# Kernel optimization log

Hardware: AMD Instinct MI355X
Metric: run time of the kernel (lower is better)

The kernel has to match this reference:

```python
import jax, jax.numpy as jnp
import numpy as np
from jax.scipy import special

B, N, DIM, H, DK, DV, F = 2, 1536, 1536, 8, 64, 64, 192


def _pos_embed(seq_len, feat):
    """Enformer relative positional basis: [2*seq_len-1, feat]."""
    per = feat // 6  # 3 basis families x (symmetric, antisymmetric)
    d = jnp.arange(-seq_len + 1, seq_len, dtype=jnp.float32)
    ad = jnp.abs(d)[:, None]  # [2N-1, 1]
    # exponential decay, log-spaced half lives
    half_life = 2.0 ** jnp.linspace(3.0, float(np.log2(seq_len)), per)
    expo = jnp.exp(-jnp.log(2.0) / half_life * ad)
    # central binary mask
    widths = 2.0 ** jnp.arange(1, per + 1, dtype=jnp.float32) - 1.0
    cmask = (widths > ad).astype(jnp.float32)
    # gamma pdf basis
    stddev = seq_len / (2.0 * per)
    start_mean = seq_len / per
    mean = jnp.linspace(start_mean, float(seq_len), per)
    conc = (mean / stddev) ** 2
    rate = mean / stddev ** 2
    log_unnorm = special.xlogy(conc - 1.0, ad) - rate * ad
    log_norm = special.gammaln(conc) - conc * jnp.log(rate)
    probs = jnp.exp(log_unnorm - log_norm) + 1e-8
    gamma = probs / jnp.max(probs, axis=-1, keepdims=True)
    emb = jnp.concatenate([expo, cmask, gamma], axis=-1)
    emb = jnp.concatenate([emb, jnp.sign(d)[:, None] * emb], axis=-1)
    return emb.astype(jnp.float32)


def _relative_shift(x):
    # x: [B, H, N, 2N-1] -> [B, H, N, N] (Transformer-XL shift)
    b, h, t1, t2 = x.shape
    x = jnp.pad(x, ((0, 0), (0, 0), (0, 0), (1, 0)))  # [B,H,N,2N]
    x = x.reshape(b, h, t2 + 1, t1)[:, :, 1:, :].reshape(b, h, t1, t2)
    return x[..., : (t2 + 2) // 2]


def setup_inputs() -> dict:
    key = jax.random.key(0)
    ks = jax.random.split(key, 8)
    s = 0.02
    return {
        "x": jax.random.normal(ks[0], (B, N, DIM), dtype=jnp.float32),
        "Wq": jax.random.normal(ks[1], (DIM, H * DK), dtype=jnp.float32) * s,
        "Wk": jax.random.normal(ks[2], (DIM, H * DK), dtype=jnp.float32) * s,
        "Wv": jax.random.normal(ks[3], (DIM, H * DV), dtype=jnp.float32) * s,
        "Wrel": jax.random.normal(ks[4], (F, H * DK), dtype=jnp.float32) * s,
        "Wout": jax.random.normal(ks[5], (H * DV, DIM), dtype=jnp.float32) * s,
        "bout": jnp.zeros((DIM,), dtype=jnp.float32),
        "rel_content_bias": jax.random.normal(ks[6], (1, H, 1, DK), dtype=jnp.float32),
        "rel_pos_bias": jax.random.normal(ks[7], (1, H, 1, DK), dtype=jnp.float32),
        "pos_embed": _pos_embed(N, F),  # [2N-1, F] buffer
    }


def reference(x, Wq, Wk, Wv, Wrel, Wout, bout, rel_content_bias, rel_pos_bias, pos_embed):
    b, n, _ = x.shape
    h, dk = rel_content_bias.shape[1], rel_content_bias.shape[3]
    dv = Wv.shape[1] // h
    scale = dk ** -0.5
    q = (x @ Wq).reshape(b, n, h, dk).transpose(0, 2, 1, 3) * scale  # [b,h,n,dk]
    k = (x @ Wk).reshape(b, n, h, dk).transpose(0, 2, 1, 3)
    v = (x @ Wv).reshape(b, n, h, dv).transpose(0, 2, 1, 3)
    content_logits = jnp.einsum('bhid,bhjd->bhij', q + rel_content_bias, k)
    rel_k = (pos_embed @ Wrel).reshape(-1, h, dk).transpose(1, 0, 2)  # [h,2n-1,dk]
    rel_logits = jnp.einsum('bhid,hjd->bhij', q + rel_pos_bias, rel_k)  # [b,h,n,2n-1]
    rel_logits = _relative_shift(rel_logits)  # [b,h,n,n]
    attn = jax.nn.softmax(content_logits + rel_logits, axis=-1)
    out = jnp.einsum('bhij,bhjd->bhid', attn, v)
    out = out.transpose(0, 2, 1, 3).reshape(b, n, h * dv)
    return out @ Wout + bout
```

## Files before the change

kernel.cpp:

```cpp
#include <hip/hip_runtime.h>

#define NSEQ  1536
#define HEADS 8
#define NREL  3071
#define NRELP 3072

typedef __bf16 bf16;
typedef __bf16 bf16x8 __attribute__((ext_vector_type(8)));
typedef __bf16 bf16x4 __attribute__((ext_vector_type(4)));
typedef float  f32x4  __attribute__((ext_vector_type(4)));

static __device__ __forceinline__ f32x4 mfma16(bf16x8 a, bf16x8 b, f32x4 c) {
  return __builtin_amdgcn_mfma_f32_16x16x32_bf16(a, b, c, 0, 0, 0);
}

static __device__ __forceinline__ void gload_lds16(const bf16* g, bf16* l) {
  __builtin_amdgcn_global_load_lds((const __attribute__((address_space(1))) void*)g,
                                   (__attribute__((address_space(3))) void*)l, 16, 0, 0);
}

#define DPP_F(v, ctrl) __int_as_float(__builtin_amdgcn_update_dpp(0, __float_as_int(v), ctrl, 0xF, 0xF, true))
static __device__ __forceinline__ float rowsum16(float v) {
  v += DPP_F(v, 0xB1);
  v += DPP_F(v, 0x4E);
  v += DPP_F(v, 0x124);
  v += DPP_F(v, 0x128);
  return v;
}

__global__ __launch_bounds__(256) void prep(const float* __restrict__ x, const float* __restrict__ pos,
                                            const float* __restrict__ Wq, const float* __restrict__ Wk,
                                            const float* __restrict__ Wv, const float* __restrict__ Wout,
                                            const float* __restrict__ Wrel,
                                            bf16* __restrict__ xb, bf16* __restrict__ posb,
                                            bf16* __restrict__ WT, bf16* __restrict__ WoT,
                                            bf16* __restrict__ WrT) {
  int blk = blockIdx.x;
  if (blk < 4608) {
    int i = blk * 256 + threadIdx.x;
    float4 v = ((const float4*)x)[i];
    bf16x4 o;
    o[0] = (bf16)v.x; o[1] = (bf16)v.y; o[2] = (bf16)v.z; o[3] = (bf16)v.w;
    ((bf16x4*)xb)[i] = o;
    return;
  }
  blk -= 4608;
  if (blk < 576) {
    int i = blk * 256 + threadIdx.x;
    if (i < (NREL * 192 / 4)) {
      float4 v = ((const float4*)pos)[i];
      bf16x4 o;
      o[0] = (bf16)v.x; o[1] = (bf16)v.y; o[2] = (bf16)v.z; o[3] = (bf16)v.w;
      ((bf16x4*)posb)[i] = o;
    }
    return;
  }
  blk -= 576;
  const float* in; bf16* out; int C, ostride, orowoff, cx, ry;
  if (blk < 768)       { in = Wq;   out = WT;  C = 512;  ostride = 1536; orowoff = 0;    cx = blk % 16; ry = blk / 16; }
  else if (blk < 1536) { blk -= 768;  in = Wk;   out = WT;  C = 512;  ostride = 1536; orowoff = 512;  cx = blk % 16; ry = blk / 16; }
  else if (blk < 2304) { blk -= 1536; in = Wv;   out = WT;  C = 512;  ostride = 1536; orowoff = 1024; cx = blk % 16; ry = blk / 16; }
  else if (blk < 3072) { blk -= 2304; in = Wout; out = WoT; C = 1536; ostride = 512;  orowoff = 0;    cx = blk % 48; ry = blk / 48; }
  else                 { blk -= 3072; in = Wrel; out = WrT; C = 512;  ostride = 192;  orowoff = 0;    cx = blk % 16; ry = blk / 16; }
  __shared__ float t[32][33];
  int tx = threadIdx.x & 31, ty = threadIdx.x >> 5;
  int r0 = ry * 32, c0 = cx * 32;
#pragma unroll
  for (int i = 0; i < 4; i++)
    t[ty + 8 * i][tx] = in[(size_t)(r0 + ty + 8 * i) * C + c0 + tx];
  __syncthreads();
#pragma unroll
  for (int i = 0; i < 4; i++)
    out[(size_t)(c0 + ty + 8 * i + orowoff) * ostride + r0 + tx] = (bf16)t[tx][ty + 8 * i];
}

static __device__ __forceinline__ void gemm_core(const bf16* __restrict__ A, const bf16* __restrict__ BT,
                                                 int Klen, int ldk, int m0, int n0, int M,
                                                 bf16* sa, bf16* sb, f32x4 acc[4][2]) {
  int tid = threadIdx.x, wave = tid >> 6, lane = tid & 63;
  int l15 = lane & 15, quad = lane >> 4;
  int lrow = lane >> 3, lcg = lane & 7;
  int swz = (lcg ^ lrow) * 8;

  int rowA = wave * 16 + lrow;
  int ra0 = m0 + rowA;     if (ra0 > M - 1) ra0 = M - 1;
  int ra1 = m0 + rowA + 8; if (ra1 > M - 1) ra1 = M - 1;
  const bf16* pA0 = A + (size_t)ra0 * ldk + swz;
  const bf16* pA1 = A + (size_t)ra1 * ldk + swz;
  int rowB = wave * 32 + lrow;
  const bf16* pB = BT + (size_t)(n0 + rowB) * ldk + swz;
  size_t ldk8 = (size_t)ldk * 8;
  bf16* wA = sa + rowA * 64 + lcg * 8;
  bf16* wB = sb + rowB * 64 + lcg * 8;

  float4 a0 = *(const float4*)pA0;
  float4 a1 = *(const float4*)pA1;
  float4 b0 = *(const float4*)(pB);
  float4 b1 = *(const float4*)(pB + ldk8);
  float4 b2 = *(const float4*)(pB + 2 * ldk8);
  float4 b3 = *(const float4*)(pB + 3 * ldk8);

  int swzA = (quad ^ (l15 & 7)) * 8;
  int swzB = ((4 + quad) ^ (l15 & 7)) * 8;

  for (int k0 = 0; k0 < Klen; k0 += 64) {
    __syncthreads();
    *(float4*)(wA) = a0;        *(float4*)(wA + 512) = a1;
    *(float4*)(wB) = b0;        *(float4*)(wB + 512) = b1;
    *(float4*)(wB + 1024) = b2; *(float4*)(wB + 1536) = b3;
    __syncthreads();
    if (k0 + 64 < Klen) {
      pA0 += 64; pA1 += 64; pB += 64;
      a0 = *(const float4*)pA0;
      a1 = *(const float4*)pA1;
      b0 = *(const float4*)(pB);
      b1 = *(const float4*)(pB + ldk8);
      b2 = *(const float4*)(pB + 2 * ldk8);
      b3 = *(const float4*)(pB + 3 * ldk8);
    }
#pragma unroll
    for (int kq = 0; kq < 2; kq++) {
      bf16x8 af[4], bfr[2];
      int sz = kq ? swzB : swzA;
#pragma unroll
      for (int rt = 0; rt < 4; rt++)
        af[rt] = *(const bf16x8*)&sa[(rt * 16 + l15) * 64 + sz];
#pragma unroll
      for (int ct = 0; ct < 2; ct++)
        bfr[ct] = *(const bf16x8*)&sb[(wave * 32 + ct * 16 + l15) * 64 + sz];
#pragma unroll
      for (int ct = 0; ct < 2; ct++)
#pragma unroll
        for (int rt = 0; rt < 4; rt++)
          acc[rt][ct] = mfma16(af[rt], bfr[ct], acc[rt][ct]);
    }
  }
}

__global__ __launch_bounds__(256) void gemm_qkvrel(const bf16* __restrict__ xb, const bf16* __restrict__ WT,
                                                   const bf16* __restrict__ posb, const bf16* __restrict__ WrT,
                                                   const float* __restrict__ cb, const float* __restrict__ pb,
                                                   bf16* __restrict__ qc, bf16* __restrict__ qp,
                                                   bf16* __restrict__ kb, bf16* __restrict__ vt,
                                                   bf16* __restrict__ rk) {
  __shared__ __align__(16) bf16 sa[64 * 64];
  __shared__ __align__(16) bf16 sb[128 * 64];
  __shared__ __align__(16) bf16 tv[64 * 130];
  int tid = threadIdx.x, wave = tid >> 6, lane = tid & 63;
  int l15 = lane & 15, quad = lane >> 4;
  int m0 = blockIdx.x * 64;
  f32x4 acc[4][2] = {};
  if (blockIdx.y >= 12) {
    int n0 = (blockIdx.y - 12) * 128;
    gemm_core(posb, WrT, 192, 192, m0, n0, NREL, sa, sb, acc);
#pragma unroll
    for (int rt = 0; rt < 4; rt++)
#pragma unroll
      for (int ct = 0; ct < 2; ct++)
#pragma unroll
        for (int r = 0; r < 4; r++) {
          int row = m0 + rt * 16 + quad * 4 + r;
          if (row < NREL) {
            int col = n0 + wave * 32 + ct * 16 + l15;
            rk[((size_t)(col >> 6) * NRELP + row) * 64 + (col & 63)] = (bf16)acc[rt][ct][r];
          }
        }
    return;
  }
  int n0 = blockIdx.y * 128;
  gemm_core(xb, WT, 1536, 1536, m0, n0, 3072, sa, sb, acc);
  int b = m0 / NSEQ, nseq0 = m0 % NSEQ;
  if (blockIdx.y < 8) {
    bool isq = blockIdx.y < 4;
#pragma unroll
    for (int rt = 0; rt < 4; rt++)
#pragma unroll
      for (int ct = 0; ct < 2; ct++)
#pragma unroll
        for (int r = 0; r < 4; r++) {
          int row = nseq0 + rt * 16 + quad * 4 + r;
          int colg = n0 + wave * 32 + ct * 16 + l15;
          int col = colg & 511;
          int h = col >> 6, d = col & 63;
          size_t o = ((size_t)(b * 8 + h) * NSEQ + row) * 64 + d;
          float v = acc[rt][ct][r];
          if (isq) {
            float qv = v * 0.18033688011f;
            qc[o] = (bf16)(qv + cb[col] * 1.44269504089f);
            qp[o] = (bf16)(qv + pb[col] * 1.44269504089f);
          } else {
            kb[o] = (bf16)v;
          }
        }
  } else {
#pragma unroll
    for (int rt = 0; rt < 4; rt++)
#pragma unroll
      for (int ct = 0; ct < 2; ct++)
#pragma unroll
        for (int r = 0; r < 4; r++)
          tv[(rt * 16 + quad * 4 + r) * 130 + wave * 32 + ct * 16 + l15] = (bf16)acc[rt][ct][r];
    __syncthreads();
    int n = tid & 63, c0v = tid >> 6;
    int hbase = (blockIdx.y - 8) * 2;
#pragma unroll
    for (int hh = 0; hh < 2; hh++)
#pragma unroll
      for (int i = 0; i < 16; i++) {
        int dv = i * 4 + c0v;
        vt[((size_t)(b * 8 + hbase + hh) * 64 + dv) * NSEQ + nseq0 + n] = tv[n * 130 + hh * 64 + dv];
      }
  }
}

__global__ __launch_bounds__(256) void gemm_out(const bf16* __restrict__ A, const bf16* __restrict__ BT,
                                                float* __restrict__ C, const float* __restrict__ bias) {
  __shared__ __align__(16) bf16 sa[64 * 64];
  __shared__ __align__(16) bf16 sb[128 * 64];
  int tid = threadIdx.x, wave = tid >> 6, lane = tid & 63;
  int l15 = lane & 15, quad = lane >> 4;
  int m0 = blockIdx.x * 64, n0 = blockIdx.y * 128;
  f32x4 acc[4][2] = {};
  gemm_core(A, BT, 512, 512, m0, n0, 3072, sa, sb, acc);
#pragma unroll
  for (int rt = 0; rt < 4; rt++)
#pragma unroll
    for (int ct = 0; ct < 2; ct++)
#pragma unroll
      for (int r = 0; r < 4; r++) {
        int row = m0 + rt * 16 + quad * 4 + r;
        int col = n0 + wave * 32 + ct * 16 + l15;
        C[(size_t)row * 1536 + col] = acc[rt][ct][r] + bias[col];
      }
}

__global__ __launch_bounds__(256, 4) void attn(const bf16* __restrict__ qc, const bf16* __restrict__ qp,
                                               const bf16* __restrict__ kb, const bf16* __restrict__ vt,
                                               const bf16* __restrict__ rk,
                                               float* __restrict__ Opart, float* __restrict__ mlp) {
  __shared__ __align__(16) bf16 sk[64 * 64];
  __shared__ __align__(16) bf16 sv[64 * 64];
  __shared__ __align__(16) bf16 srel[128 * 64];
  __shared__ __align__(16) bf16 pls[4][16 * 64];
  int qb = blockIdx.x, bh = blockIdx.y, kz = blockIdx.z;
  int h = bh & 7;
  int i0 = qb * 64;
  int wave = threadIdx.x >> 6, lane = threadIdx.x & 63;
  int l15 = lane & 15, quad = lane >> 4;
  int lrow = lane >> 3, lcg = lane & 7;
  const bf16* qcb = qc + (size_t)bh * NSEQ * 64;
  const bf16* qpb = qp + (size_t)bh * NSEQ * 64;
  const bf16* kbb = kb + (size_t)bh * NSEQ * 64;
  const bf16* vtb = vt + (size_t)bh * 64 * NSEQ;
  const bf16* rkh = rk + (size_t)h * NRELP * 64;
  bf16* plsw = pls[wave];

  int qrow = i0 + wave * 16 + l15;
  bf16x8 aqc0 = *(const bf16x8*)(qcb + (size_t)qrow * 64 + quad * 8);
  bf16x8 aqc1 = *(const bf16x8*)(qcb + (size_t)qrow * 64 + 32 + quad * 8);
  bf16x8 aqp0 = *(const bf16x8*)(qpb + (size_t)qrow * 64 + quad * 8);
  bf16x8 aqp1 = *(const bf16x8*)(qpb + (size_t)qrow * 64 + 32 + quad * 8);

  int bidx[4];
  bool hisel[4];
#pragma unroll
  for (int r = 0; r < 4; r++) {
    int rl = quad * 4 + r;
    bidx[r] = (quad * 16 + ((l15 + 15 - rl) & 15)) << 2;
    hisel[r] = l15 > rl;
  }

  int swz = (lcg ^ lrow) * 8;
  int jb = 23 + kz * 12 - qb;
  const bf16* pK = kbb + (size_t)(kz * 768 + wave * 16 + lrow) * 64 + swz;
  const bf16* pV = vtb + (size_t)(wave * 16 + lrow) * NSEQ + kz * 768 + swz;
  const bf16* pR = rkh + (size_t)(jb + 1) * 4096 + (size_t)(wave * 16 + lrow) * 64 + swz;
  bf16* wK = sk + (wave * 16 + lrow) * 64 + lcg * 8;
  bf16* wV = sv + (wave * 16 + lrow) * 64 + lcg * 8;
  int wRoff = (wave * 16 + lrow) * 64 + lcg * 8;

  {
    const bf16* pP = rkh + (size_t)jb * 4096 + (size_t)(wave * 16 + lrow) * 64 + swz;
    bf16* dP = srel + ((jb & 1) * 64 + wave * 16) * 64;
#pragma unroll
    for (int t = 0; t < 2; t++)
      gload_lds16(pP + t * 512, dP + t * 512);
  }
  float4 kr0 = *(const float4*)(pK), kr1 = *(const float4*)(pK + 512);             pK += 4096;
  float4 vr0 = *(const float4*)(pV), vr1 = *(const float4*)(pV + 8 * NSEQ);        pV += 64;
  float4 rr0 = *(const float4*)(pR), rr1 = *(const float4*)(pR + 512);             pR += 4096;
  int pxor = (jb & 1) << 6;

  int swzA = (quad ^ (l15 & 7)) * 8;
  int swzB = ((4 + quad) ^ (l15 & 7)) * 8;
  int rb0 = (3 - wave) * 16 + l15;
  int pxl = (l15 >> 1) << 3;
  const bf16* plr = plsw + l15 * 64;

  f32x4 acco[4] = {};
  float li[4] = {0.0f, 0.0f, 0.0f, 0.0f};

  for (int jt = 0; jt < 12; jt++) {
    __syncthreads();
    *(float4*)(wK) = kr0;        *(float4*)(wK + 512) = kr1;
    *(float4*)(wV) = vr0;        *(float4*)(wV + 512) = vr1;
    {
      bf16* wR = srel + (pxor ^ 64) * 64 + wRoff;
      *(float4*)(wR) = rr0;      *(float4*)(wR + 512) = rr1;
    }
    __syncthreads();
    if (jt < 11) {
      kr0 = *(const float4*)(pK); kr1 = *(const float4*)(pK + 512);        pK += 4096;
      vr0 = *(const float4*)(pV); vr1 = *(const float4*)(pV + 8 * NSEQ);   pV += 64;
      rr0 = *(const float4*)(pR); rr1 = *(const float4*)(pR + 512);        pR += 4096;
    }
    f32x4 s[4] = {};
#pragma unroll
    for (int c = 0; c < 4; c++) {
      const bf16* kp = sk + (c * 16 + l15) * 64;
      s[c] = mfma16(aqc0, *(const bf16x8*)(kp + swzA), s[c]);
      s[c] = mfma16(aqc1, *(const bf16x8*)(kp + swzB), s[c]);
    }
    f32x4 sb5[5];
#pragma unroll
    for (int cc = 0; cc < 5; cc++) {
      const bf16* rp = srel + ((rb0 + cc * 16) ^ pxor) * 64;
      f32x4 z = {};
      z = mfma16(aqp0, *(const bf16x8*)(rp + swzA), z);
      sb5[cc] = mfma16(aqp1, *(const bf16x8*)(rp + swzB), z);
    }
#pragma unroll
    for (int r = 0; r < 4; r++) {
      float bp[5];
#pragma unroll
      for (int cc = 0; cc < 5; cc++)
        bp[cc] = __int_as_float(__builtin_amdgcn_ds_bpermute(bidx[r], __float_as_int(sb5[cc][r])));
#pragma unroll
      for (int c = 0; c < 4; c++)
        s[c][r] += hisel[r] ? bp[c + 1] : bp[c];
    }
#pragma unroll
    for (int c = 0; c < 4; c++)
#pragma unroll
      for (int r = 0; r < 4; r++) {
        float p = __builtin_amdgcn_exp2f(s[c][r] - 11.5415603f);
        bf16 pbh = (bf16)p;
        li[r] += (float)pbh;
        int prow = quad * 4 + r;
        plsw[prow * 64 + ((c * 16 + l15) ^ ((prow >> 1) << 3))] = pbh;
      }
#pragma unroll
    for (int ks = 0; ks < 2; ks++) {
      bf16x8 ap = *(const bf16x8*)(plr + ((ks * 32 + quad * 8) ^ pxl));
#pragma unroll
      for (int c = 0; c < 4; c++) {
        const bf16* vp = sv + (c * 16 + l15) * 64;
        acco[c] = mfma16(ap, *(const bf16x8*)(vp + (ks ? swzB : swzA)), acco[c]);
      }
    }
    pxor ^= 64;
  }
#pragma unroll
  for (int r = 0; r < 4; r++)
    li[r] = rowsum16(li[r]);
  int qt16 = qb * 4 + wave;
  size_t pbase = ((size_t)(bh * 96 + qt16) * 2 + kz);
#pragma unroll
  for (int c = 0; c < 4; c++)
#pragma unroll
    for (int r = 0; r < 4; r++)
      Opart[pbase * 1024 + (quad * 4 + r) * 64 + c * 16 + l15] = acco[c][r];
  if (l15 == 0) {
#pragma unroll
    for (int r = 0; r < 4; r++)
      mlp[pbase * 16 + quad * 4 + r] = li[r];
  }
}

__global__ void attn_merge(const float* __restrict__ Opart, const float* __restrict__ mlp,
                           bf16* __restrict__ O) {
  int qt = blockIdx.x, bh = blockIdx.y;
  int b = bh >> 3, h = bh & 7;
  int col = threadIdx.x & 63, rg = threadIdx.x >> 6;
  size_t base = (size_t)(bh * 96 + qt) * 2;
#pragma unroll
  for (int rr = 0; rr < 4; rr++) {
    int row = rg * 4 + rr;
    float L = mlp[base * 16 + row] + mlp[(base + 1) * 16 + row];
    float v = Opart[base * 1024 + row * 64 + col] + Opart[(base + 1) * 1024 + row * 64 + col];
    O[((size_t)(b * NSEQ + qt * 16 + row) * 8 + h) * 64 + col] = (bf16)(v / L);
  }
}

extern "C" void kernel_launch(void* const* d_in, const int* in_sizes, int n_in,
                              void* d_out, int out_size, void* d_ws, size_t ws_size,
                              hipStream_t stream) {
  const float* x    = (const float*)d_in[0];
  const float* Wq   = (const float*)d_in[1];
  const float* Wk   = (const float*)d_in[2];
  const float* Wv   = (const float*)d_in[3];
  const float* Wrel = (const float*)d_in[4];
  const float* Wout = (const float*)d_in[5];
  const float* bout = (const float*)d_in[6];
  const float* cb   = (const float*)d_in[7];
  const float* pb   = (const float*)d_in[8];
  const float* pos  = (const float*)d_in[9];
  float* out = (float*)d_out;

  char* ws = (char*)d_ws;
  size_t off = 0;
  auto alloc = [&](size_t bytes) {
    char* p = ws + off;
    off = (off + bytes + 255) & ~(size_t)255;
    return p;
  };
  bf16*  xb    = (bf16*)alloc(3072UL * 1536 * 2);
  bf16*  WT    = (bf16*)alloc(1536UL * 1536 * 2);
  bf16*  WoT   = (bf16*)alloc(1536UL * 512 * 2);
  bf16*  WrT   = (bf16*)alloc(512UL * 192 * 2);
  bf16*  posb  = (bf16*)alloc((size_t)NREL * 192 * 2);
  bf16*  qcb   = (bf16*)alloc(16UL * NSEQ * 64 * 2);
  bf16*  qpb   = (bf16*)alloc(16UL * NSEQ * 64 * 2);
  bf16*  kbb   = (bf16*)alloc(16UL * NSEQ * 64 * 2);
  bf16*  vtb   = (bf16*)alloc(16UL * NSEQ * 64 * 2);
  bf16*  rkb   = (bf16*)alloc(8UL * NRELP * 64 * 2);
  bf16*  Ob    = (bf16*)alloc(3072UL * 512 * 2);
  float* Opart = (float*)alloc(16UL * 96 * 2 * 1024 * 4);
  float* mlpw  = (float*)alloc(16UL * 96 * 2 * 16 * 4);

  prep<<<dim3(8352), 256, 0, stream>>>(x, pos, Wq, Wk, Wv, Wout, Wrel, xb, posb, WT, WoT, WrT);
  gemm_qkvrel<<<dim3(48, 16), 256, 0, stream>>>(xb, WT, posb, WrT, cb, pb, qcb, qpb, kbb, vtb, rkb);
  attn<<<dim3(24, 16, 2), 256, 0, stream>>>(qcb, qpb, kbb, vtb, rkb, Opart, mlpw);
  attn_merge<<<dim3(96, 16), 256, 0, stream>>>(Opart, mlpw, Ob);
  gemm_out<<<dim3(48, 12), 256, 0, stream>>>(Ob, WoT, out, bout);
}
```

Before: 174.4 us.

## Use 128x128 eight-wave GEMM tiles with direct global-to-LDS loads

```diff
diff --git a/kernel.cpp b/kernel.cpp
--- a/kernel.cpp
+++ b/kernel.cpp
@@ -74,12 +74,13 @@
     out[(size_t)(c0 + ty + 8 * i + orowoff) * ostride + r0 + tx] = (bf16)t[tx][ty + 8 * i];
 }
 
-static __device__ __forceinline__ void gemm_core(const bf16* __restrict__ A, const bf16* __restrict__ BT,
-                                                 int Klen, int ldk, int m0, int n0, int M,
-                                                 bf16* sa, bf16* sb, f32x4 acc[4][2]) {
+static __device__ __forceinline__ void gemm_core8(const bf16* __restrict__ A, const bf16* __restrict__ BT,
+                                                  int Klen, int ldk, int m0, int n0, int M,
+                                                  bf16* sa, bf16* sb, f32x4 acc[4][2]) {
   int tid = threadIdx.x, wave = tid >> 6, lane = tid & 63;
   int l15 = lane & 15, quad = lane >> 4;
   int lrow = lane >> 3, lcg = lane & 7;
+  int wr = wave >> 2, wc = wave & 3;
   int swz = (lcg ^ lrow) * 8;
 
   int rowA = wave * 16 + lrow;
@@ -87,47 +88,33 @@
   int ra1 = m0 + rowA + 8; if (ra1 > M - 1) ra1 = M - 1;
   const bf16* pA0 = A + (size_t)ra0 * ldk + swz;
   const bf16* pA1 = A + (size_t)ra1 * ldk + swz;
-  int rowB = wave * 32 + lrow;
-  const bf16* pB = BT + (size_t)(n0 + rowB) * ldk + swz;
-  size_t ldk8 = (size_t)ldk * 8;
-  bf16* wA = sa + rowA * 64 + lcg * 8;
-  bf16* wB = sb + rowB * 64 + lcg * 8;
-
-  float4 a0 = *(const float4*)pA0;
-  float4 a1 = *(const float4*)pA1;
-  float4 b0 = *(const float4*)(pB);
-  float4 b1 = *(const float4*)(pB + ldk8);
-  float4 b2 = *(const float4*)(pB + 2 * ldk8);
-  float4 b3 = *(const float4*)(pB + 3 * ldk8);
+  const bf16* pB0 = BT + (size_t)(n0 + rowA) * ldk + swz;
+  const bf16* pB1 = BT + (size_t)(n0 + rowA + 8) * ldk + swz;
+  bf16* dA = sa + (wave * 16) * 64;
+  bf16* dB = sb + (wave * 16) * 64;
 
   int swzA = (quad ^ (l15 & 7)) * 8;
   int swzB = ((4 + quad) ^ (l15 & 7)) * 8;
+  const bf16* ar = sa + (wr * 64 + l15) * 64;
+  const bf16* br = sb + (wc * 32 + l15) * 64;
 
   for (int k0 = 0; k0 < Klen; k0 += 64) {
     __syncthreads();
-    *(float4*)(wA) = a0;        *(float4*)(wA + 512) = a1;
-    *(float4*)(wB) = b0;        *(float4*)(wB + 512) = b1;
-    *(float4*)(wB + 1024) = b2; *(float4*)(wB + 1536) = b3;
-    __syncthreads();
-    if (k0 + 64 < Klen) {
-      pA0 += 64; pA1 += 64; pB += 64;
-      a0 = *(const float4*)pA0;
-      a1 = *(const float4*)pA1;
-      b0 = *(const float4*)(pB);
-      b1 = *(const float4*)(pB + ldk8);
-      b2 = *(const float4*)(pB + 2 * ldk8);
-      b3 = *(const float4*)(pB + 3 * ldk8);
-    }
+    gload_lds16(pA0 + k0, dA);
+    gload_lds16(pA1 + k0, dA + 512);
+    gload_lds16(pB0 + k0, dB);
+    gload_lds16(pB1 + k0, dB + 512);
+    __syncthreads();
 #pragma unroll
     for (int kq = 0; kq < 2; kq++) {
       bf16x8 af[4], bfr[2];
       int sz = kq ? swzB : swzA;
 #pragma unroll
       for (int rt = 0; rt < 4; rt++)
-        af[rt] = *(const bf16x8*)&sa[(rt * 16 + l15) * 64 + sz];
+        af[rt] = *(const bf16x8*)&ar[rt * 16 * 64 + sz];
 #pragma unroll
       for (int ct = 0; ct < 2; ct++)
-        bfr[ct] = *(const bf16x8*)&sb[(wave * 32 + ct * 16 + l15) * 64 + sz];
+        bfr[ct] = *(const bf16x8*)&br[ct * 16 * 64 + sz];
 #pragma unroll
       for (int ct = 0; ct < 2; ct++)
 #pragma unroll
@@ -137,38 +124,40 @@
   }
 }
 
-__global__ __launch_bounds__(256) void gemm_qkvrel(const bf16* __restrict__ xb, const bf16* __restrict__ WT,
+__global__ __launch_bounds__(512) void gemm_qkvrel(const bf16* __restrict__ xb, const bf16* __restrict__ WT,
                                                    const bf16* __restrict__ posb, const bf16* __restrict__ WrT,
                                                    const float* __restrict__ cb, const float* __restrict__ pb,
                                                    bf16* __restrict__ qc, bf16* __restrict__ qp,
                                                    bf16* __restrict__ kb, bf16* __restrict__ vt,
                                                    bf16* __restrict__ rk) {
-  __shared__ __align__(16) bf16 sa[64 * 64];
-  __shared__ __align__(16) bf16 sb[128 * 64];
-  __shared__ __align__(16) bf16 tv[64 * 130];
+  __shared__ __align__(16) bf16 smem[16640];
+  bf16* sa = smem;
+  bf16* sb = smem + 8192;
+  bf16* tv = smem;
   int tid = threadIdx.x, wave = tid >> 6, lane = tid & 63;
   int l15 = lane & 15, quad = lane >> 4;
-  int m0 = blockIdx.x * 64;
+  int wr = wave >> 2, wc = wave & 3;
+  int m0 = blockIdx.x * 128;
   f32x4 acc[4][2] = {};
   if (blockIdx.y >= 12) {
     int n0 = (blockIdx.y - 12) * 128;
-    gemm_core(posb, WrT, 192, 192, m0, n0, NREL, sa, sb, acc);
+    gemm_core8(posb, WrT, 192, 192, m0, n0, NREL, sa, sb, acc);
 #pragma unroll
     for (int rt = 0; rt < 4; rt++)
 #pragma unroll
       for (int ct = 0; ct < 2; ct++)
 #pragma unroll
         for (int r = 0; r < 4; r++) {
-          int row = m0 + rt * 16 + quad * 4 + r;
+          int row = m0 + wr * 64 + rt * 16 + quad * 4 + r;
           if (row < NREL) {
-            int col = n0 + wave * 32 + ct * 16 + l15;
+            int col = n0 + wc * 32 + ct * 16 + l15;
             rk[((size_t)(col >> 6) * NRELP + row) * 64 + (col & 63)] = (bf16)acc[rt][ct][r];
           }
         }
     return;
   }
   int n0 = blockIdx.y * 128;
-  gemm_core(xb, WT, 1536, 1536, m0, n0, 3072, sa, sb, acc);
+  gemm_core8(xb, WT, 1536, 1536, m0, n0, 3072, sa, sb, acc);
   int b = m0 / NSEQ, nseq0 = m0 % NSEQ;
   if (blockIdx.y < 8) {
     bool isq = blockIdx.y < 4;
@@ -178,8 +167,8 @@
       for (int ct = 0; ct < 2; ct++)
 #pragma unroll
         for (int r = 0; r < 4; r++) {
-          int row = nseq0 + rt * 16 + quad * 4 + r;
-          int colg = n0 + wave * 32 + ct * 16 + l15;
+          int row = nseq0 + wr * 64 + rt * 16 + quad * 4 + r;
+          int colg = n0 + wc * 32 + ct * 16 + l15;
           int col = colg & 511;
           int h = col >> 6, d = col & 63;
           size_t o = ((size_t)(b * 8 + h) * NSEQ + row) * 64 + d;
@@ -193,43 +182,44 @@
           }
         }
   } else {
+    __syncthreads();
 #pragma unroll
     for (int rt = 0; rt < 4; rt++)
 #pragma unroll
       for (int ct = 0; ct < 2; ct++)
 #pragma unroll
         for (int r = 0; r < 4; r++)
-          tv[(rt * 16 + quad * 4 + r) * 130 + wave * 32 + ct * 16 + l15] = (bf16)acc[rt][ct][r];
-    __syncthreads();
-    int n = tid & 63, c0v = tid >> 6;
+          tv[(wr * 64 + rt * 16 + quad * 4 + r) * 130 + wc * 32 + ct * 16 + l15] = (bf16)acc[rt][ct][r];
+    __syncthreads();
+    int n = tid & 127, cq = tid >> 7;
     int hbase = (blockIdx.y - 8) * 2;
 #pragma unroll
-    for (int hh = 0; hh < 2; hh++)
-#pragma unroll
-      for (int i = 0; i < 16; i++) {
-        int dv = i * 4 + c0v;
-        vt[((size_t)(b * 8 + hbase + hh) * 64 + dv) * NSEQ + nseq0 + n] = tv[n * 130 + hh * 64 + dv];
-      }
-  }
-}
-
-__global__ __launch_bounds__(256) void gemm_out(const bf16* __restrict__ A, const bf16* __restrict__ BT,
+    for (int i = 0; i < 32; i++) {
+      int dvl = i * 4 + cq;
+      int hh = dvl >> 6, dv = dvl & 63;
+      vt[((size_t)(b * 8 + hbase + hh) * 64 + dv) * NSEQ + nseq0 + n] = tv[n * 130 + dvl];
+    }
+  }
+}
+
+__global__ __launch_bounds__(512) void gemm_out(const bf16* __restrict__ A, const bf16* __restrict__ BT,
                                                 float* __restrict__ C, const float* __restrict__ bias) {
-  __shared__ __align__(16) bf16 sa[64 * 64];
+  __shared__ __align__(16) bf16 sa[128 * 64];
   __shared__ __align__(16) bf16 sb[128 * 64];
   int tid = threadIdx.x, wave = tid >> 6, lane = tid & 63;
   int l15 = lane & 15, quad = lane >> 4;
-  int m0 = blockIdx.x * 64, n0 = blockIdx.y * 128;
+  int wr = wave >> 2, wc = wave & 3;
+  int m0 = blockIdx.x * 128, n0 = blockIdx.y * 128;
   f32x4 acc[4][2] = {};
-  gemm_core(A, BT, 512, 512, m0, n0, 3072, sa, sb, acc);
+  gemm_core8(A, BT, 512, 512, m0, n0, 3072, sa, sb, acc);
 #pragma unroll
   for (int rt = 0; rt < 4; rt++)
 #pragma unroll
     for (int ct = 0; ct < 2; ct++)
 #pragma unroll
       for (int r = 0; r < 4; r++) {
-        int row = m0 + rt * 16 + quad * 4 + r;
-        int col = n0 + wave * 32 + ct * 16 + l15;
+        int row = m0 + wr * 64 + rt * 16 + quad * 4 + r;
+        int col = n0 + wc * 32 + ct * 16 + l15;
         C[(size_t)row * 1536 + col] = acc[rt][ct][r] + bias[col];
       }
 }
@@ -429,8 +419,8 @@
   float* mlpw  = (float*)alloc(16UL * 96 * 2 * 16 * 4);
 
   prep<<<dim3(8352), 256, 0, stream>>>(x, pos, Wq, Wk, Wv, Wout, Wrel, xb, posb, WT, WoT, WrT);
-  gemm_qkvrel<<<dim3(48, 16), 256, 0, stream>>>(xb, WT, posb, WrT, cb, pb, qcb, qpb, kbb, vtb, rkb);
+  gemm_qkvrel<<<dim3(24, 16), 512, 0, stream>>>(xb, WT, posb, WrT, cb, pb, qcb, qpb, kbb, vtb, rkb);
   attn<<<dim3(24, 16, 2), 256, 0, stream>>>(qcb, qpb, kbb, vtb, rkb, Opart, mlpw);
   attn_merge<<<dim3(96, 16), 256, 0, stream>>>(Opart, mlpw, Ob);
-  gemm_out<<<dim3(48, 12), 256, 0, stream>>>(Ob, WoT, out, bout);
-}
+  gemm_out<<<dim3(24, 12), 512, 0, stream>>>(Ob, WoT, out, bout);
+}
```

After: 174.8 us. Within noise of the previous version (+0.2%).
